# Kernel optimization log

Measured on AMD Instinct MI355X. Metric: run time of the kernel, lower is better.

## Reference

```python
import jax, jax.numpy as jnp
import numpy as np

B, C, P, L = 128, 5, 5, 5
D = 128
USER_NUM, TITLE_NUM, ENTITY_NUM, REL_NUM = 50000, 30000, 100000, 100


def setup_inputs() -> dict:
    key = jax.random.key(0)
    k = jax.random.split(key, 22)
    f = jnp.float32
    s = 0.1  # weight scale to keep LSTM gates in a sane range
    return {
        "candidate_newsindex": jax.random.randint(k[0], (B, C), 0, TITLE_NUM),
        "user_index": jax.random.randint(k[1], (B,), 0, USER_NUM),
        "total_paths_index": jax.random.randint(k[2], (USER_NUM, C, P, L), 0, TITLE_NUM),
        "total_type_index": jax.random.randint(k[3], (USER_NUM, C, P, L), 0, 3),
        "total_relations_index": jax.random.randint(k[4], (USER_NUM, C, P, L), 0, REL_NUM),
        "entity_emb": jax.random.normal(k[5], (ENTITY_NUM, D), f),
        "relation_emb": jax.random.normal(k[6], (REL_NUM, D), f),
        "user_emb": jax.random.normal(k[7], (USER_NUM, D), f),
        "news_emb": jax.random.normal(k[8], (TITLE_NUM, D), f),
        "type_emb": jax.random.normal(k[9], (3, D), f),
        "Wih0": jax.random.normal(k[10], (P, 4 * D, 3 * D), f) * s,
        "Whh0": jax.random.normal(k[11], (P, 4 * D, D), f) * s,
        "bih0": jax.random.normal(k[12], (P, 4 * D), f) * s,
        "bhh0": jax.random.normal(k[13], (P, 4 * D), f) * s,
        "Wih1": jax.random.normal(k[14], (P, 4 * D, D), f) * s,
        "Whh1": jax.random.normal(k[15], (P, 4 * D, D), f) * s,
        "bih1": jax.random.normal(k[16], (P, 4 * D), f) * s,
        "bhh1": jax.random.normal(k[17], (P, 4 * D), f) * s,
        "W1": jax.random.normal(k[18], (16, D), f) * s,
        "b1": jax.random.normal(k[19], (16,), f) * s,
        "W2": jax.random.normal(k[20], (1, 16), f) * s,
        "b2": jax.random.normal(k[21], (1,), f) * s,
    }


def _lstm2(x, Wih0, Whh0, bih0, bhh0, Wih1, Whh1, bih1, bhh1):
    """2-layer PyTorch-style LSTM (gate order i,f,g,o). x: [N, T, in] -> [N, T, H]."""
    def layer(x, Wih, Whh, bih, bhh):
        N = x.shape[0]
        H = Whh.shape[1]
        h0 = jnp.zeros((N, H), x.dtype)
        c0 = jnp.zeros((N, H), x.dtype)
        b = bih + bhh
        def step(carry, xt):
            h, c = carry
            g = xt @ Wih.T + h @ Whh.T + b
            i, f, gg, o = jnp.split(g, 4, axis=-1)
            c = jax.nn.sigmoid(f) * c + jax.nn.sigmoid(i) * jnp.tanh(gg)
            h = jax.nn.sigmoid(o) * jnp.tanh(c)
            return (h, c), h
        _, ys = jax.lax.scan(step, (h0, c0), x.swapaxes(0, 1))
        return ys.swapaxes(0, 1)
    x = layer(x, Wih0, Whh0, bih0, bhh0)
    x = layer(x, Wih1, Whh1, bih1, bhh1)
    return x


def reference(candidate_newsindex, user_index, total_paths_index, total_type_index,
              total_relations_index, entity_emb, relation_emb, user_emb, news_emb,
              type_emb, Wih0, Whh0, bih0, bhh0, Wih1, Whh1, bih1, bhh1,
              W1, b1, W2, b2):
    bpath = total_paths_index[user_index]  # [B,C,P,L]
    btype = total_type_index[user_index]
    brel = total_relations_index[user_index]
    # per-node embedding selected by type: 0->user, 1->news, else entity
    node = jnp.where((btype == 0)[..., None], user_emb[bpath],
                     jnp.where((btype == 1)[..., None], news_emb[bpath], entity_emb[bpath]))
    inp = jnp.concatenate([node, type_emb[btype], relation_emb[brel]], axis=-1)  # [B,C,P,L,3D]
    Bb, Cc, Pp, Ll, F = inp.shape
    x = inp.transpose(2, 0, 1, 3, 4).reshape(Pp, Bb * Cc, Ll, F)  # per-path batches
    outs = jax.vmap(_lstm2)(x, Wih0, Whh0, bih0, bhh0, Wih1, Whh1, bih1, bhh1)  # [P,BC,L,H]
    idx = jnp.arange(Pp)
    sel = outs[idx, :, idx, :]  # LSTM i's output at timestep i -> [P, BC, H]
    ps = jax.nn.sigmoid(jnp.maximum(sel @ W1.T + b1, 0.0) @ W2.T + b2)[..., 0]  # [P,BC]
    ps_mean = ps.reshape(Pp, Bb, Cc).mean(axis=0)  # [B,C]
    # faithful to source: total_output accumulates over candidates j, so the score
    # for candidate j is the cumulative mean of path scores for candidates 0..j
    total_score = jnp.cumsum(ps_mean, axis=1) / jnp.arange(1, Cc + 1, dtype=ps_mean.dtype)
    emb_score = jax.nn.sigmoid(jnp.sum(news_emb[candidate_newsindex] * user_emb[user_index][:, None, :], axis=-1))
    return emb_score + total_score
```

## Files before the change

### kernel.cpp

```cpp
#include <hip/hip_runtime.h>
#include <math.h>

#define BB   128
#define CC   5
#define PP   5
#define LL   5
#define DD   128
#define NSEQ 640
#define GATES 512
#define IN0  384
#define HPAD 136

typedef __attribute__((ext_vector_type(8))) short short8;
typedef __attribute__((ext_vector_type(4))) float f32x4;
typedef __attribute__((address_space(1))) const unsigned int as1_uint;
typedef __attribute__((address_space(3))) unsigned int as3_uint;

__device__ __forceinline__ float sigf(float x){ return 1.0f/(1.0f+__expf(-x)); }
__device__ __forceinline__ float tanhfast(float x){ return 1.0f - 2.0f/(__expf(2.0f*x)+1.0f); }

__device__ __forceinline__ unsigned short f2bf(float x){
    union { float f; unsigned u; } v; v.f = x;
    unsigned r = v.u + 0x7FFF + ((v.u >> 16) & 1);
    return (unsigned short)(r >> 16);
}

__device__ __constant__ int c_ptmap[15] = {0,5,6,10,11,12,15,16,17,18,20,21,22,23,24};

__global__ void stage0_kernel(const float* __restrict__ Wih0, const float* __restrict__ Whh0,
                              const float* __restrict__ Wih1, const float* __restrict__ Whh1,
                              const float* __restrict__ bih0, const float* __restrict__ bhh0,
                              const float* __restrict__ bih1, const float* __restrict__ bhh1,
                              unsigned short* __restrict__ F0, unsigned short* __restrict__ F1,
                              unsigned short* __restrict__ F2, unsigned short* __restrict__ F3,
                              float* __restrict__ b0, float* __restrict__ b1c,
                              float* __restrict__ psum,
                              const int* __restrict__ user_index,
                              const int* __restrict__ tpath, const int* __restrict__ ttype,
                              const int* __restrict__ trel,
                              const float* __restrict__ entity_emb, const float* __restrict__ relation_emb,
                              const float* __restrict__ user_emb, const float* __restrict__ news_emb,
                              const float* __restrict__ type_emb,
                              unsigned short* __restrict__ X,
                              const int* __restrict__ cand,
                              float* __restrict__ embv, int* __restrict__ ctr){
    int bx = blockIdx.x;
    if (bx < 985){
        int id = bx*256 + threadIdx.x;
        const int NF0 = PP*12*32*64;
        const int NFH = PP*4*32*64;
        if (id < NF0 + 3*NFH){
            const float* src; unsigned short* dst; int K, KT, fid;
            if (id < NF0){ src = Wih0; dst = F0; K = IN0; KT = 12; fid = id; }
            else {
                int j = id - NF0; int m = j / NFH; fid = j % NFH; K = DD; KT = 4;
                src = (m==0)?Whh0:(m==1)?Wih1:Whh1;
                dst = (m==0)?F1:(m==1)?F2:F3;
            }
            int lane = fid & 63; int rem = fid >> 6;
            int gt = rem & 31; rem >>= 5;
            int kt = rem % KT; int p = rem / KT;
            int g  = gt*16 + (lane & 15);
            int k0 = kt*32 + (lane >> 4)*8;
            const float* s = src + (size_t)(p*GATES + g)*K + k0;
            float4 x0 = *(const float4*)s;
            float4 x1 = *(const float4*)(s+4);
            uint4 o;
            o.x = f2bf(x0.x) | ((unsigned)f2bf(x0.y)<<16);
            o.y = f2bf(x0.z) | ((unsigned)f2bf(x0.w)<<16);
            o.z = f2bf(x1.x) | ((unsigned)f2bf(x1.y)<<16);
            o.w = f2bf(x1.z) | ((unsigned)f2bf(x1.w)<<16);
            *(uint4*)(dst + (size_t)fid*8) = o;
        } else {
            int j = id - (NF0 + 3*NFH);
            if (j < PP*GATES) b0[j] = bih0[j] + bhh0[j];
            else if (j < 2*PP*GATES){ int q = j - PP*GATES; b1c[q] = bih1[q] + bhh1[q]; }
            else if (j < 2*PP*GATES + NSEQ){ psum[j - 2*PP*GATES] = 0.0f; }
            else if (j == 2*PP*GATES + NSEQ){ ctr[0] = 0; }
        }
    } else if (bx < 2785){
        int id = (bx - 985)*256 + threadIdx.x;
        if (id >= 15*NSEQ*48) return;
        int ptIdx = id / (NSEQ*48); int rem = id % (NSEQ*48);
        int n = rem / 48, q = rem % 48;
        int pt = c_ptmap[ptIdx];
        int p = pt / LL, t = pt % LL;
        int b = n / CC, c = n % CC;
        int u = user_index[b];
        int base = ((u*CC + c)*PP + p)*LL + t;
        int col = q*8;
        const float* s;
        if (q < 16){
            int ty = ttype[base]; int pi = tpath[base];
            const float* e = (ty==0)?user_emb:(ty==1)?news_emb:entity_emb;
            s = e + (size_t)pi*DD + col;
        } else if (q < 32){
            s = type_emb + (size_t)ttype[base]*DD + (col-128);
        } else {
            s = relation_emb + (size_t)trel[base]*DD + (col-256);
        }
        float4 x0 = *(const float4*)s, x1 = *(const float4*)(s+4);
        uint4 o;
        o.x = f2bf(x0.x) | ((unsigned)f2bf(x0.y)<<16);
        o.y = f2bf(x0.z) | ((unsigned)f2bf(x0.w)<<16);
        o.z = f2bf(x1.x) | ((unsigned)f2bf(x1.y)<<16);
        o.w = f2bf(x1.z) | ((unsigned)f2bf(x1.w)<<16);
        *(uint4*)(X + (size_t)(pt*NSEQ + n)*IN0 + col) = o;
    } else {
        int id = (bx - 2785)*256 + threadIdx.x;
        int n = id >> 4, k = id & 15;
        int b = n / CC;
        int nb = cand[n];
        int u = user_index[b];
        const float4* ne = (const float4*)(news_emb + (size_t)nb*DD + k*8);
        const float4* ue = (const float4*)(user_emb + (size_t)u*DD + k*8);
        float4 a0 = ne[0], a1 = ne[1], u0 = ue[0], u1 = ue[1];
        float v = a0.x*u0.x + a0.y*u0.y + a0.z*u0.z + a0.w*u0.w
                + a1.x*u1.x + a1.y*u1.y + a1.z*u1.z + a1.w*u1.w;
        #pragma unroll
        for (int off=8; off; off>>=1) v += __shfl_down(v, off, 16);
        if (k == 0) embv[n] = v;
    }
}

__global__ __launch_bounds__(256) void gemm_ih0_v5(const unsigned short* __restrict__ X,
                                                   const unsigned short* __restrict__ F0,
                                                   float* __restrict__ G0c){
    __shared__ unsigned short Bs[12*4*512];
    int bx = blockIdx.x;
    int nch = bx & 7;
    int m64 = (bx >> 3) % 10;
    int pt  = c_ptmap[bx / 80];
    int p = pt / LL;
    int tid = threadIdx.x, lane = tid & 63, w = tid >> 6;
    int r16 = lane & 15, qd = lane >> 4;

    const unsigned short* Fp = F0 + (((size_t)p*12)*32 + nch*4)*512;
    uint4 breg[12];
    #pragma unroll
    for (int j=0;j<12;j++)
        breg[j] = *(const uint4*)(Fp + (size_t)j*32*512 + tid*8);
    #pragma unroll
    for (int j=0;j<12;j++)
        *(uint4*)(Bs + j*2048 + tid*8) = breg[j];
    __syncthreads();

    f32x4 acc[4];
    #pragma unroll
    for (int i=0;i<4;i++) acc[i] = (f32x4)0.0f;
    const unsigned short* Xb = X + ((size_t)pt*NSEQ + m64*64 + w*16 + r16)*IN0 + qd*8;
    #pragma unroll
    for (int kt=0; kt<12; kt++){
        short8 a = *(const short8*)(Xb + kt*32);
        #pragma unroll
        for (int i=0;i<4;i++){
            short8 bfr = *(const short8*)(Bs + (kt*4+i)*512 + lane*8);
            acc[i] = __builtin_amdgcn_mfma_f32_16x16x32_bf16(a, bfr, acc[i], 0,0,0);
        }
    }
    int tile16 = pt*40 + m64*4 + w;
    float* dst = G0c + (((size_t)tile16*32 + nch*4)*64 + lane)*4;
    #pragma unroll
    for (int i=0;i<4;i++)
        *(f32x4*)(dst + (size_t)i*256) = acc[i];
}

__global__ __launch_bounds__(512, 2) void lstm_v8(
    const float* __restrict__ G0c,
    const unsigned short* __restrict__ F1,
    const unsigned short* __restrict__ F2,
    const unsigned short* __restrict__ F3,
    const float* __restrict__ b0, const float* __restrict__ b1c,
    const float* __restrict__ W1, const float* __restrict__ b1v,
    const float* __restrict__ W2, const float* __restrict__ b2v,
    float* __restrict__ psum,
    const float* __restrict__ embv, int* __restrict__ ctr,
    float* __restrict__ out){
    __shared__ __align__(16) unsigned short F1s[4*32*512];
    __shared__ unsigned short h0T[2][16*HPAD];
    __shared__ unsigned short h1T[2][16*HPAD];
    __shared__ int lastFlag;
    float* h1f  = (float*)F1s;
    float* mlpb = (float*)(F1s + 16*132*2);

    int p = blockIdx.x / 40, nt = blockIdx.x % 40;
    int n0 = nt*16;
    int tid = threadIdx.x;
    int lane = tid & 63, w = tid >> 6;
    int r16 = lane & 15, qd = lane >> 4;
    int j = w*16 + r16;

    if (p > 0){
        const unsigned short* F1g = F1 + (size_t)p*4*32*512;
        #pragma unroll
        for (int v=0; v<16; v++){
            __builtin_amdgcn_global_load_lds(
                (as1_uint*)(F1g + (size_t)v*4096 + tid*8),
                (as3_uint*)(F1s + v*4096 + (tid & 448)*8),
                16, 0, 0);
        }
    }

    short8 f2r[16], f3r[16];
    {
        const unsigned short* F2p = F2 + (size_t)p*4*32*512 + lane*8;
        const unsigned short* F3p = F3 + (size_t)p*4*32*512 + lane*8;
        #pragma unroll
        for (int kt=0; kt<4; kt++)
            #pragma unroll
            for (int i=0;i<4;i++){
                f2r[kt*4+i] = *(const short8*)(F2p + (size_t)(kt*32 + i*8 + w)*512);
                f3r[kt*4+i] = *(const short8*)(F3p + (size_t)(kt*32 + i*8 + w)*512);
            }
    }
    float bL0[4], bL1[4];
    #pragma unroll
    for (int i=0;i<4;i++){
        int col = (i*8 + w)*16 + r16;
        bL0[i] = b0[p*GATES + col];
        bL1[i] = b1c[p*GATES + col];
    }

    f32x4 pf[4];
    {
        const float* slab = G0c + (size_t)((p*LL + 0)*40 + nt)*8192;
        #pragma unroll
        for (int i=0;i<4;i++) pf[i] = *(const f32x4*)(slab + ((i*8+w)*64 + lane)*4);
    }
    float c0s[4] = {0,0,0,0}, c1s[4] = {0,0,0,0};

    for (int t=0; t<=p; t++){
        const int cur = t & 1, prv = cur ^ 1;
        f32x4 acc[4];
        #pragma unroll
        for (int i=0;i<4;i++){
            f32x4 a = pf[i]; float bb = bL0[i];
            a[0]+=bb; a[1]+=bb; a[2]+=bb; a[3]+=bb; acc[i]=a;
        }
        if (t < p){
            const float* ns = G0c + (size_t)((p*LL + t + 1)*40 + nt)*8192;
            #pragma unroll
            for (int i=0;i<4;i++) pf[i] = *(const f32x4*)(ns + ((i*8+w)*64 + lane)*4);
        }
        if (t > 0){
            #pragma unroll
            for (int kt=0; kt<4; kt++){
                short8 a = *(const short8*)(&h0T[prv][0] + r16*HPAD + kt*32 + qd*8);
                #pragma unroll
                for (int i=0;i<4;i++){
                    short8 bfr = *(const short8*)(F1s + (size_t)(kt*32 + i*8 + w)*512 + lane*8);
                    acc[i] = __builtin_amdgcn_mfma_f32_16x16x32_bf16(a, bfr, acc[i], 0,0,0);
                }
            }
        }
        #pragma unroll
        for (int v=0; v<4; v++){
            float cc = sigf(acc[1][v])*c0s[v] + sigf(acc[0][v])*tanhfast(acc[2][v]);
            c0s[v] = cc;
            h0T[cur][(qd*4+v)*HPAD + j] = f2bf(sigf(acc[3][v])*tanhfast(cc));
        }
        __syncthreads();
        #pragma unroll
        for (int i=0;i<4;i++){
            float bb = bL1[i];
            f32x4 a; a[0]=bb; a[1]=bb; a[2]=bb; a[3]=bb; acc[i]=a;
        }
        #pragma unroll
        for (int kt=0; kt<4; kt++){
            short8 a = *(const short8*)(&h0T[cur][0] + r16*HPAD + kt*32 + qd*8);
            #pragma unroll
            for (int i=0;i<4;i++)
                acc[i] = __builtin_amdgcn_mfma_f32_16x16x32_bf16(a, f2r[kt*4+i], acc[i], 0,0,0);
        }
        if (t > 0){
            #pragma unroll
            for (int kt=0; kt<4; kt++){
                short8 a = *(const short8*)(&h1T[prv][0] + r16*HPAD + kt*32 + qd*8);
                #pragma unroll
                for (int i=0;i<4;i++)
                    acc[i] = __builtin_amdgcn_mfma_f32_16x16x32_bf16(a, f3r[kt*4+i], acc[i], 0,0,0);
            }
        }
        #pragma unroll
        for (int v=0; v<4; v++){
            float cc = sigf(acc[1][v])*c1s[v] + sigf(acc[0][v])*tanhfast(acc[2][v]);
            c1s[v] = cc;
            float hh = sigf(acc[3][v])*tanhfast(cc);
            if (t < p) h1T[cur][(qd*4+v)*HPAD + j] = f2bf(hh);
            else       h1f[(qd*4+v)*132 + j] = hh;
        }
    }
    __syncthreads();
    if (tid < 256){
        int rr = tid & 15, hc = tid >> 4;
        const float4* w1r = (const float4*)(W1 + hc*DD);
        const float4* hrow = (const float4*)(h1f + rr*132);
        float a0 = b1v[hc], a1 = 0.0f, a2 = 0.0f, a3 = 0.0f;
        #pragma unroll
        for (int k=0;k<32;k++){
            float4 wv = w1r[k];
            float4 hv = hrow[k];
            a0 = fmaf(hv.x, wv.x, a0);
            a1 = fmaf(hv.y, wv.y, a1);
            a2 = fmaf(hv.z, wv.z, a2);
            a3 = fmaf(hv.w, wv.w, a3);
        }
        mlpb[hc*17 + rr] = fmaxf((a0+a1)+(a2+a3), 0.0f);
    }
    __syncthreads();
    if (tid < 16){
        float s = b2v[0];
        #pragma unroll
        for (int h=0;h<16;h++) s = fmaf(mlpb[h*17 + tid], W2[h], s);
        atomicAdd(&psum[n0 + tid], 0.2f*sigf(s));
        __threadfence();
    }
    __syncthreads();
    if (tid == 0){
        int old = atomicAdd(ctr, 1);
        lastFlag = (old == 199);
    }
    __syncthreads();
    if (!lastFlag) return;
    float* ps = (float*)F1s;
    for (int i = tid; i < NSEQ; i += 512)
        ps[i] = atomicAdd(&psum[i], 0.0f);
    __syncthreads();
    if (tid < BB){
        float cum = 0.0f;
        #pragma unroll
        for (int c=0;c<CC;c++){
            cum += ps[tid*CC + c];
            out[tid*CC + c] = sigf(embv[tid*CC + c]) + cum/(float)(c+1);
        }
    }
}

extern "C" void kernel_launch(void* const* d_in, const int* in_sizes, int n_in,
                              void* d_out, int out_size, void* d_ws, size_t ws_size,
                              hipStream_t stream){
    const int* cand        = (const int*)d_in[0];
    const int* uidx        = (const int*)d_in[1];
    const int* tpath       = (const int*)d_in[2];
    const int* ttype       = (const int*)d_in[3];
    const int* trel        = (const int*)d_in[4];
    const float* entity_emb   = (const float*)d_in[5];
    const float* relation_emb = (const float*)d_in[6];
    const float* user_emb     = (const float*)d_in[7];
    const float* news_emb     = (const float*)d_in[8];
    const float* type_emb     = (const float*)d_in[9];
    const float* Wih0 = (const float*)d_in[10];
    const float* Whh0 = (const float*)d_in[11];
    const float* bih0 = (const float*)d_in[12];
    const float* bhh0 = (const float*)d_in[13];
    const float* Wih1 = (const float*)d_in[14];
    const float* Whh1 = (const float*)d_in[15];
    const float* bih1 = (const float*)d_in[16];
    const float* bhh1 = (const float*)d_in[17];
    const float* W1 = (const float*)d_in[18];
    const float* b1 = (const float*)d_in[19];
    const float* W2 = (const float*)d_in[20];
    const float* b2 = (const float*)d_in[21];
    float* out = (float*)d_out;

    char* ws = (char*)d_ws;
    unsigned short* F0 = (unsigned short*)ws;  ws += (size_t)PP*12*32*512*2;
    unsigned short* F1 = (unsigned short*)ws;  ws += (size_t)PP*4*32*512*2;
    unsigned short* F2 = (unsigned short*)ws;  ws += (size_t)PP*4*32*512*2;
    unsigned short* F3 = (unsigned short*)ws;  ws += (size_t)PP*4*32*512*2;
    float* b0  = (float*)ws;                   ws += PP*GATES*4;
    float* b1c = (float*)ws;                   ws += PP*GATES*4;
    unsigned short* X = (unsigned short*)ws;   ws += (size_t)PP*LL*NSEQ*IN0*2;
    float* G0c = (float*)ws;                   ws += (size_t)PP*LL*NSEQ*GATES*4;
    float* psum = (float*)ws;                  ws += NSEQ*4;
    float* embv = (float*)ws;                  ws += NSEQ*4;
    int*   ctr  = (int*)ws;                    ws += 4;

    stage0_kernel<<<985+1800+40,256,0,stream>>>(Wih0,Whh0,Wih1,Whh1,bih0,bhh0,bih1,bhh1,
                                             F0,F1,F2,F3,b0,b1c,psum,
                                             uidx,tpath,ttype,trel,entity_emb,relation_emb,
                                             user_emb,news_emb,type_emb,X,
                                             cand,embv,ctr);
    gemm_ih0_v5<<<1200,256,0,stream>>>(X, F0, G0c);
    lstm_v8<<<200,512,0,stream>>>(G0c, F1, F2, F3, b0, b1c, W1, b1, W2, b2,
                                  psum, embv, ctr, out);
}
```

Measured before the change: 221.4 us.

## Fuse three stage kernels into one cooperative mega-kernel with grid syncs

Replaces the three separate launches (prep/gather, input GEMM, LSTM recurrence) with a single cooperative kernel of 200 blocks that runs the same phases separated by grid-wide syncs, and does the final score combine in block 0. The aim is to remove launch gaps and inter-kernel drain between stages. The cost is that the prep and GEMM phases now run on only 200 blocks instead of thousands, and each grid.sync adds latency. If the cooperative launch fails, the code falls back to the old three-kernel path.

After: 327.4 us. +47.9%, slower.

```diff
diff --git a/kernel.cpp b/kernel.cpp
--- a/kernel.cpp
+++ b/kernel.cpp
@@ -1,5 +1,8 @@
 #include <hip/hip_runtime.h>
+#include <hip/hip_cooperative_groups.h>
 #include <math.h>
+
+namespace cg = cooperative_groups;
 
 #define BB   128
 #define CC   5
@@ -26,6 +29,309 @@
 }
 
 __device__ __constant__ int c_ptmap[15] = {0,5,6,10,11,12,15,16,17,18,20,21,22,23,24};
+
+__global__ __launch_bounds__(512, 2) void mega_kernel(
+    const float* __restrict__ Wih0, const float* __restrict__ Whh0,
+    const float* __restrict__ Wih1, const float* __restrict__ Whh1,
+    const float* __restrict__ bih0, const float* __restrict__ bhh0,
+    const float* __restrict__ bih1, const float* __restrict__ bhh1,
+    unsigned short* __restrict__ F0, unsigned short* __restrict__ F1,
+    unsigned short* __restrict__ F2, unsigned short* __restrict__ F3,
+    float* __restrict__ b0, float* __restrict__ b1c,
+    float* __restrict__ psum,
+    const int* __restrict__ user_index,
+    const int* __restrict__ tpath, const int* __restrict__ ttype,
+    const int* __restrict__ trel,
+    const float* __restrict__ entity_emb, const float* __restrict__ relation_emb,
+    const float* __restrict__ user_emb, const float* __restrict__ news_emb,
+    const float* __restrict__ type_emb,
+    unsigned short* __restrict__ X, const int* __restrict__ cand,
+    float* __restrict__ embv,
+    const float* __restrict__ W1, const float* __restrict__ b1v,
+    const float* __restrict__ W2, const float* __restrict__ b2v,
+    float* __restrict__ G0c, float* __restrict__ out)
+{
+    __shared__ __align__(16) unsigned short F1s[4*32*512];
+    __shared__ unsigned short h0T[2][16*HPAD];
+    __shared__ unsigned short h1T[2][16*HPAD];
+
+    cg::grid_group grid = cg::this_grid();
+    int bx = blockIdx.x, tid = threadIdx.x;
+    int lane = tid & 63, w = tid >> 6;
+    int r16 = lane & 15, qd = lane >> 4;
+
+    const int P1 = 985*256;
+    const int P2 = P1 + 15*NSEQ*48;
+    const int NTOT = P2 + NSEQ*16;
+    for (int it = bx*512 + tid; it < NTOT; it += 200*512){
+        if (it < P1){
+            int id = it;
+            const int NF0 = PP*12*32*64;
+            const int NFH = PP*4*32*64;
+            if (id < NF0 + 3*NFH){
+                const float* src; unsigned short* dst; int K, KT, fid;
+                if (id < NF0){ src = Wih0; dst = F0; K = IN0; KT = 12; fid = id; }
+                else {
+                    int jx = id - NF0; int m = jx / NFH; fid = jx % NFH; K = DD; KT = 4;
+                    src = (m==0)?Whh0:(m==1)?Wih1:Whh1;
+                    dst = (m==0)?F1:(m==1)?F2:F3;
+                }
+                int ln = fid & 63; int rem = fid >> 6;
+                int gt = rem & 31; rem >>= 5;
+                int kt = rem % KT; int p = rem / KT;
+                int g  = gt*16 + (ln & 15);
+                int k0 = kt*32 + (ln >> 4)*8;
+                const float* s = src + (size_t)(p*GATES + g)*K + k0;
+                float4 x0 = *(const float4*)s;
+                float4 x1 = *(const float4*)(s+4);
+                uint4 o;
+                o.x = f2bf(x0.x) | ((unsigned)f2bf(x0.y)<<16);
+                o.y = f2bf(x0.z) | ((unsigned)f2bf(x0.w)<<16);
+                o.z = f2bf(x1.x) | ((unsigned)f2bf(x1.y)<<16);
+                o.w = f2bf(x1.z) | ((unsigned)f2bf(x1.w)<<16);
+                *(uint4*)(dst + (size_t)fid*8) = o;
+            } else {
+                int jx = id - (NF0 + 3*NFH);
+                if (jx < PP*GATES) b0[jx] = bih0[jx] + bhh0[jx];
+                else if (jx < 2*PP*GATES){ int q = jx - PP*GATES; b1c[q] = bih1[q] + bhh1[q]; }
+                else if (jx < 2*PP*GATES + NSEQ){ psum[jx - 2*PP*GATES] = 0.0f; }
+            }
+        } else if (it < P2){
+            int id = it - P1;
+            int ptIdx = id / (NSEQ*48); int rem = id % (NSEQ*48);
+            int n = rem / 48, q = rem % 48;
+            int pt = c_ptmap[ptIdx];
+            int p = pt / LL, t = pt % LL;
+            int b = n / CC, c = n % CC;
+            int u = user_index[b];
+            int base = ((u*CC + c)*PP + p)*LL + t;
+            int col = q*8;
+            const float* s;
+            if (q < 16){
+                int ty = ttype[base]; int pi = tpath[base];
+                const float* e = (ty==0)?user_emb:(ty==1)?news_emb:entity_emb;
+                s = e + (size_t)pi*DD + col;
+            } else if (q < 32){
+                s = type_emb + (size_t)ttype[base]*DD + (col-128);
+            } else {
+                s = relation_emb + (size_t)trel[base]*DD + (col-256);
+            }
+            float4 x0 = *(const float4*)s, x1 = *(const float4*)(s+4);
+            uint4 o;
+            o.x = f2bf(x0.x) | ((unsigned)f2bf(x0.y)<<16);
+            o.y = f2bf(x0.z) | ((unsigned)f2bf(x0.w)<<16);
+            o.z = f2bf(x1.x) | ((unsigned)f2bf(x1.y)<<16);
+            o.w = f2bf(x1.z) | ((unsigned)f2bf(x1.w)<<16);
+            *(uint4*)(X + (size_t)(pt*NSEQ + n)*IN0 + col) = o;
+        } else {
+            int id = it - P2;
+            int n = id >> 4, k = id & 15;
+            int b = n / CC;
+            int nb = cand[n];
+            int u = user_index[b];
+            const float4* ne = (const float4*)(news_emb + (size_t)nb*DD + k*8);
+            const float4* ue = (const float4*)(user_emb + (size_t)u*DD + k*8);
+            float4 a0 = ne[0], a1 = ne[1], u0 = ue[0], u1 = ue[1];
+            float v = a0.x*u0.x + a0.y*u0.y + a0.z*u0.z + a0.w*u0.w
+                    + a1.x*u1.x + a1.y*u1.y + a1.z*u1.z + a1.w*u1.w;
+            #pragma unroll
+            for (int off=8; off; off>>=1) v += __shfl_down(v, off, 16);
+            if (k == 0) embv[n] = v;
+        }
+    }
+    grid.sync();
+
+    {
+        unsigned short* Bs = F1s;
+        int curcid = -1;
+        int half = tid >> 8;
+        int t255 = tid & 255;
+        #pragma unroll
+        for (int ii=0; ii<3; ii++){
+            int T = bx*3 + ii;
+            int cid = T/5, m128 = T%5;
+            int ptIdx = cid >> 3, nch = cid & 7;
+            int pt = c_ptmap[ptIdx];
+            int p = pt / LL;
+            if (cid != curcid){
+                __syncthreads();
+                const unsigned short* Fp = F0 + (((size_t)p*12)*32 + nch*4)*512;
+                #pragma unroll
+                for (int v=0; v<6; v++){
+                    int jj = v*2 + half;
+                    __builtin_amdgcn_global_load_lds(
+                        (as1_uint*)(Fp + (size_t)jj*32*512 + t255*8),
+                        (as3_uint*)(Bs + jj*2048 + (t255 & 192)*8),
+                        16, 0, 0);
+                }
+                __syncthreads();
+                curcid = cid;
+            }
+            f32x4 acc[4];
+            #pragma unroll
+            for (int i=0;i<4;i++) acc[i] = (f32x4)0.0f;
+            const unsigned short* Xb = X + ((size_t)pt*NSEQ + m128*128 + w*16 + r16)*IN0 + qd*8;
+            #pragma unroll
+            for (int kt=0; kt<12; kt++){
+                short8 a = *(const short8*)(Xb + kt*32);
+                #pragma unroll
+                for (int i=0;i<4;i++){
+                    short8 bfr = *(const short8*)(Bs + (kt*4+i)*512 + lane*8);
+                    acc[i] = __builtin_amdgcn_mfma_f32_16x16x32_bf16(a, bfr, acc[i], 0,0,0);
+                }
+            }
+            int tile16 = pt*40 + m128*8 + w;
+            float* dst = G0c + (((size_t)tile16*32 + nch*4)*64 + lane)*4;
+            #pragma unroll
+            for (int i=0;i<4;i++)
+                *(f32x4*)(dst + (size_t)i*256) = acc[i];
+        }
+    }
+    grid.sync();
+
+    {
+        float* h1f  = (float*)F1s;
+        float* mlpb = (float*)(F1s + 16*132*2);
+        int pL = bx / 40, nt = bx % 40;
+        int n0 = nt*16;
+        int j = w*16 + r16;
+
+        if (pL > 0){
+            const unsigned short* F1g = F1 + (size_t)pL*4*32*512;
+            #pragma unroll
+            for (int v=0; v<16; v++){
+                __builtin_amdgcn_global_load_lds(
+                    (as1_uint*)(F1g + (size_t)v*4096 + tid*8),
+                    (as3_uint*)(F1s + v*4096 + (tid & 448)*8),
+                    16, 0, 0);
+            }
+        }
+
+        short8 f2r[16], f3r[16];
+        {
+            const unsigned short* F2p = F2 + (size_t)pL*4*32*512 + lane*8;
+            const unsigned short* F3p = F3 + (size_t)pL*4*32*512 + lane*8;
+            #pragma unroll
+            for (int kt=0; kt<4; kt++)
+                #pragma unroll
+                for (int i=0;i<4;i++){
+                    f2r[kt*4+i] = *(const short8*)(F2p + (size_t)(kt*32 + i*8 + w)*512);
+                    f3r[kt*4+i] = *(const short8*)(F3p + (size_t)(kt*32 + i*8 + w)*512);
+                }
+        }
+        float bL0[4], bL1[4];
+        #pragma unroll
+        for (int i=0;i<4;i++){
+            int col = (i*8 + w)*16 + r16;
+            bL0[i] = b0[pL*GATES + col];
+            bL1[i] = b1c[pL*GATES + col];
+        }
+
+        f32x4 pf[4];
+        {
+            const float* slab = G0c + (size_t)((pL*LL + 0)*40 + nt)*8192;
+            #pragma unroll
+            for (int i=0;i<4;i++) pf[i] = *(const f32x4*)(slab + ((i*8+w)*64 + lane)*4);
+        }
+        float c0s[4] = {0,0,0,0}, c1s[4] = {0,0,0,0};
+
+        for (int t=0; t<=pL; t++){
+            const int cur = t & 1, prv = cur ^ 1;
+            f32x4 acc[4];
+            #pragma unroll
+            for (int i=0;i<4;i++){
+                f32x4 a = pf[i]; float bb = bL0[i];
+                a[0]+=bb; a[1]+=bb; a[2]+=bb; a[3]+=bb; acc[i]=a;
+            }
+            if (t < pL){
+                const float* ns = G0c + (size_t)((pL*LL + t + 1)*40 + nt)*8192;
+                #pragma unroll
+                for (int i=0;i<4;i++) pf[i] = *(const f32x4*)(ns + ((i*8+w)*64 + lane)*4);
+            }
+            if (t > 0){
+                #pragma unroll
+                for (int kt=0; kt<4; kt++){
+                    short8 a = *(const short8*)(&h0T[prv][0] + r16*HPAD + kt*32 + qd*8);
+                    #pragma unroll
+                    for (int i=0;i<4;i++){
+                        short8 bfr = *(const short8*)(F1s + (size_t)(kt*32 + i*8 + w)*512 + lane*8);
+                        acc[i] = __builtin_amdgcn_mfma_f32_16x16x32_bf16(a, bfr, acc[i], 0,0,0);
+                    }
+                }
+            }
+            #pragma unroll
+            for (int v=0; v<4; v++){
+                float cc = sigf(acc[1][v])*c0s[v] + sigf(acc[0][v])*tanhfast(acc[2][v]);
+                c0s[v] = cc;
+                h0T[cur][(qd*4+v)*HPAD + j] = f2bf(sigf(acc[3][v])*tanhfast(cc));
+            }
+            __syncthreads();
+            #pragma unroll
+            for (int i=0;i<4;i++){
+                float bb = bL1[i];
+                f32x4 a; a[0]=bb; a[1]=bb; a[2]=bb; a[3]=bb; acc[i]=a;
+            }
+            #pragma unroll
+            for (int kt=0; kt<4; kt++){
+                short8 a = *(const short8*)(&h0T[cur][0] + r16*HPAD + kt*32 + qd*8);
+                #pragma unroll
+                for (int i=0;i<4;i++)
+                    acc[i] = __builtin_amdgcn_mfma_f32_16x16x32_bf16(a, f2r[kt*4+i], acc[i], 0,0,0);
+            }
+            if (t > 0){
+                #pragma unroll
+                for (int kt=0; kt<4; kt++){
+                    short8 a = *(const short8*)(&h1T[prv][0] + r16*HPAD + kt*32 + qd*8);
+                    #pragma unroll
+                    for (int i=0;i<4;i++)
+                        acc[i] = __builtin_amdgcn_mfma_f32_16x16x32_bf16(a, f3r[kt*4+i], acc[i], 0,0,0);
+                }
+            }
+            #pragma unroll
+            for (int v=0; v<4; v++){
+                float cc = sigf(acc[1][v])*c1s[v] + sigf(acc[0][v])*tanhfast(acc[2][v]);
+                c1s[v] = cc;
+                float hh = sigf(acc[3][v])*tanhfast(cc);
+                if (t < pL) h1T[cur][(qd*4+v)*HPAD + j] = f2bf(hh);
+                else        h1f[(qd*4+v)*132 + j] = hh;
+            }
+        }
+        __syncthreads();
+        if (tid < 256){
+            int rr = tid & 15, hc = tid >> 4;
+            const float4* w1r = (const float4*)(W1 + hc*DD);
+            const float4* hrow = (const float4*)(h1f + rr*132);
+            float a0 = b1v[hc], a1 = 0.0f, a2 = 0.0f, a3 = 0.0f;
+            #pragma unroll
+            for (int k=0;k<32;k++){
+                float4 wv = w1r[k];
+                float4 hv = hrow[k];
+                a0 = fmaf(hv.x, wv.x, a0);
+                a1 = fmaf(hv.y, wv.y, a1);
+                a2 = fmaf(hv.z, wv.z, a2);
+                a3 = fmaf(hv.w, wv.w, a3);
+            }
+            mlpb[hc*17 + rr] = fmaxf((a0+a1)+(a2+a3), 0.0f);
+        }
+        __syncthreads();
+        if (tid < 16){
+            float s = b2v[0];
+            #pragma unroll
+            for (int h=0;h<16;h++) s = fmaf(mlpb[h*17 + tid], W2[h], s);
+            atomicAdd(&psum[n0 + tid], 0.2f*sigf(s));
+        }
+    }
+    grid.sync();
+
+    if (bx == 0 && tid < BB){
+        float cum = 0.0f;
+        #pragma unroll
+        for (int c=0;c<CC;c++){
+            cum += psum[tid*CC + c];
+            out[tid*CC + c] = sigf(embv[tid*CC + c]) + cum/(float)(c+1);
+        }
+    }
+}
 
 __global__ void stage0_kernel(const float* __restrict__ Wih0, const float* __restrict__ Whh0,
                               const float* __restrict__ Wih1, const float* __restrict__ Whh1,
@@ -376,12 +682,29 @@
     float* embv = (float*)ws;                  ws += NSEQ*4;
     int*   ctr  = (int*)ws;                    ws += 4;
 
-    stage0_kernel<<<985+1800+40,256,0,stream>>>(Wih0,Whh0,Wih1,Whh1,bih0,bhh0,bih1,bhh1,
-                                             F0,F1,F2,F3,b0,b1c,psum,
-                                             uidx,tpath,ttype,trel,entity_emb,relation_emb,
-                                             user_emb,news_emb,type_emb,X,
-                                             cand,embv,ctr);
-    gemm_ih0_v5<<<1200,256,0,stream>>>(X, F0, G0c);
-    lstm_v8<<<200,512,0,stream>>>(G0c, F1, F2, F3, b0, b1c, W1, b1, W2, b2,
-                                  psum, embv, ctr, out);
+    void* kargs[] = {
+        (void*)&Wih0, (void*)&Whh0, (void*)&Wih1, (void*)&Whh1,
+        (void*)&bih0, (void*)&bhh0, (void*)&bih1, (void*)&bhh1,
+        (void*)&F0, (void*)&F1, (void*)&F2, (void*)&F3,
+        (void*)&b0, (void*)&b1c, (void*)&psum,
+        (void*)&uidx, (void*)&tpath, (void*)&ttype, (void*)&trel,
+        (void*)&entity_emb, (void*)&relation_emb, (void*)&user_emb,
+        (void*)&news_emb, (void*)&type_emb,
+        (void*)&X, (void*)&cand, (void*)&embv,
+        (void*)&W1, (void*)&b1, (void*)&W2, (void*)&b2,
+        (void*)&G0c, (void*)&out
+    };
+    hipError_t err = hipLaunchCooperativeKernel((void*)mega_kernel,
+                                                dim3(200), dim3(512),
+                                                kargs, 0, stream);
+    if (err != hipSuccess){
+        stage0_kernel<<<985+1800+40,256,0,stream>>>(Wih0,Whh0,Wih1,Whh1,bih0,bhh0,bih1,bhh1,
+                                                 F0,F1,F2,F3,b0,b1c,psum,
+                                                 uidx,tpath,ttype,trel,entity_emb,relation_emb,
+                                                 user_emb,news_emb,type_emb,X,
+                                                 cand,embv,ctr);
+        gemm_ih0_v5<<<1200,256,0,stream>>>(X, F0, G0c);
+        lstm_v8<<<200,512,0,stream>>>(G0c, F1, F2, F3, b0, b1c, W1, b1, W2, b2,
+                                      psum, embv, ctr, out);
+    }
 }
```
